# Kernel optimization log

Hardware: AMD Instinct MI355X
Metric: run time of the kernel (lower is better)

The kernel has to match this reference:

```python
import jax, jax.numpy as jnp
import numpy as np

D, H, W = 96, 160, 160
N_FLOWS = 3
RANGE_FLOW = 0.4


def make_base_grid():
    # torch.meshgrid over arange per dim, stacked: [1, 3, D, H, W], channel order (d, h, w)
    zz, yy, xx = jnp.meshgrid(jnp.arange(D), jnp.arange(H), jnp.arange(W), indexing='ij')
    return jnp.stack([zz, yy, xx]).astype(jnp.float32)[None]


def normalize_grid(g):
    # g: [1,3,D,H,W] voxel coords (d,h,w). Apply 2*(v/(s-1) - 0.5), permute to
    # channels-last and reverse channel order -> (x,y,z) as grid_sample expects.
    scale = jnp.array([2.0 / (D - 1), 2.0 / (H - 1), 2.0 / (W - 1)], jnp.float32).reshape(1, 3, 1, 1, 1)
    g = g * scale - 1.0
    return jnp.moveaxis(g, 1, -1)[..., ::-1]  # [1,D,H,W,3], xyz


def grid_sample_3d(img, grid):
    # Trilinear grid_sample, align_corners=False, zeros padding (torch defaults).
    # img: [N,C,D,H,W]; grid: [N,D,H,W,3] with (x,y,z) in [-1,1].
    N, C, Di, Hi, Wi = img.shape
    x = ((grid[..., 0] + 1.0) * Wi - 1.0) * 0.5
    y = ((grid[..., 1] + 1.0) * Hi - 1.0) * 0.5
    z = ((grid[..., 2] + 1.0) * Di - 1.0) * 0.5
    x0 = jnp.floor(x); y0 = jnp.floor(y); z0 = jnp.floor(z)
    tx = x - x0; ty = y - y0; tz = z - z0
    x0i = x0.astype(jnp.int32); y0i = y0.astype(jnp.int32); z0i = z0.astype(jnp.int32)

    gather = jax.vmap(lambda im, a, b, c: im[:, a, b, c])  # per-batch [C,D,H,W] gather

    out = jnp.zeros((N, C) + x.shape[1:], img.dtype)
    for dz in (0, 1):
        for dy in (0, 1):
            for dx in (0, 1):
                xi = x0i + dx; yi = y0i + dy; zi = z0i + dz
                w = ((tx if dx else 1.0 - tx) * (ty if dy else 1.0 - ty) * (tz if dz else 1.0 - tz))
                valid = ((xi >= 0) & (xi < Wi) & (yi >= 0) & (yi < Hi) & (zi >= 0) & (zi < Di))
                xi = jnp.clip(xi, 0, Wi - 1); yi = jnp.clip(yi, 0, Hi - 1); zi = jnp.clip(zi, 0, Di - 1)
                vals = gather(img, zi, yi, xi)  # [N,C,D,H,W]
                out = out + vals * (w * valid)[:, None]
    return out


def setup_inputs() -> dict:
    key = jax.random.key(0)
    k1, k2, k3 = jax.random.split(key, 3)
    src = jax.random.normal(k1, (1, 1, D, H, W), jnp.float32)
    flow_list = jax.random.normal(k2, (N_FLOWS, 1, 3, D, H, W), jnp.float32)
    final_flow = jax.random.normal(k3, (1, 3, D, H, W), jnp.float32)
    range_flow = jnp.float32(RANGE_FLOW)
    return {"src": src, "flow_list": flow_list, "final_flow": final_flow, "range_flow": range_flow}


def reference(src, flow_list, final_flow, range_flow):
    base = make_base_grid()  # [1,3,D,H,W]
    flows = [flow_list[i] for i in range(flow_list.shape[0])] + [final_flow]
    composed = flows[0]
    warped = composed
    for dvf in flows[1:]:
        grid2 = normalize_grid(base + dvf * range_flow)
        warped = grid_sample_3d(composed, grid2)  # warp running composition by dvf
        composed = warped + dvf
    out_flow = warped + final_flow  # == final composed dvf
    new_locs = normalize_grid(base + composed * range_flow)
    deform_2_img = grid_sample_3d(src, new_locs)
    return (deform_2_img, out_flow)
```

## Files before the change

### kernel.cpp

```cpp
#include <hip/hip_runtime.h>

constexpr int Dd  = 96;
constexpr int Hh  = 160;
constexpr int Ww  = 160;
constexpr int HW  = Hh * Ww;
constexpr int DHW = Dd * HW;
constexpr int NBLK  = DHW / 256;
constexpr int CHUNK = NBLK / 8;

__device__ __forceinline__ int swz_block(int b) {
    return (b & 7) * CHUNK + (b >> 3);
}

__device__ __forceinline__ float remap_z(float v) { return v * ((float)Dd / (float)(Dd - 1)) - 0.5f; }
__device__ __forceinline__ float remap_y(float v) { return v * ((float)Hh / (float)(Hh - 1)) - 0.5f; }
__device__ __forceinline__ float remap_x(float v) { return v * ((float)Ww / (float)(Ww - 1)) - 0.5f; }

__device__ __forceinline__ void tri_setup(float x, float y, float z,
                                          int off[8], float wgt[8]) {
    float xf = floorf(x), yf = floorf(y), zf = floorf(z);
    float tx = x - xf, ty = y - yf, tz = z - zf;
    int x0 = (int)xf, y0 = (int)yf, z0 = (int)zf;
    float wx[2] = {1.0f - tx, tx};
    float wy[2] = {1.0f - ty, ty};
    float wz[2] = {1.0f - tz, tz};
    int k = 0;
#pragma unroll
    for (int dz = 0; dz < 2; ++dz) {
        int zi = z0 + dz;
        bool vz = (zi >= 0) && (zi < Dd);
        int zc = min(max(zi, 0), Dd - 1);
#pragma unroll
        for (int dy = 0; dy < 2; ++dy) {
            int yi = y0 + dy;
            bool vy = (yi >= 0) && (yi < Hh);
            int yc = min(max(yi, 0), Hh - 1);
#pragma unroll
            for (int dx = 0; dx < 2; ++dx) {
                int xi = x0 + dx;
                bool vx = (xi >= 0) && (xi < Ww);
                int xc = min(max(xi, 0), Ww - 1);
                float w = wz[dz] * wy[dy] * wx[dx];
                wgt[k] = (vx && vy && vz) ? w : 0.0f;
                off[k] = zc * HW + yc * Ww + xc;
                ++k;
            }
        }
    }
}

__global__ __launch_bounds__(256) void pack3to4(
        const float* __restrict__ f, float4* __restrict__ out)
{
    int idx = blockIdx.x * blockDim.x + threadIdx.x;
    out[idx] = make_float4(f[idx], f[DHW + idx], f[2 * DHW + idx], 0.0f);
}

__global__ __launch_bounds__(256) void warp_compose4(
        const float4* __restrict__ composed,
        const float* __restrict__ dvf,
        const float* __restrict__ rf_ptr,
        float4* __restrict__ out4)
{
    int idx = swz_block(blockIdx.x) * 256 + threadIdx.x;
    float rf = *rf_ptr;

    int d = idx / HW;
    int rem = idx - d * HW;
    int h = rem / Ww;
    int w = rem - h * Ww;

    float fd = dvf[idx];
    float fh = dvf[DHW + idx];
    float fw = dvf[2 * DHW + idx];

    float z = remap_z((float)d + fd * rf);
    float y = remap_y((float)h + fh * rf);
    float x = remap_x((float)w + fw * rf);

    int off[8]; float wgt[8];
    tri_setup(x, y, z, off, wgt);

    float a0 = 0.0f, a1 = 0.0f, a2 = 0.0f;
#pragma unroll
    for (int k = 0; k < 8; ++k) {
        float4 v = composed[off[k]];
        float wk = wgt[k];
        a0 += wk * v.x;
        a1 += wk * v.y;
        a2 += wk * v.z;
    }
    out4[idx] = make_float4(a0 + fd, a1 + fh, a2 + fw, 0.0f);
}

__global__ __launch_bounds__(256) void warp_final_fused(
        const float4* __restrict__ composed2,
        const float* __restrict__ fflow,
        const float* __restrict__ src,
        const float* __restrict__ rf_ptr,
        float* __restrict__ out_flow,
        float* __restrict__ out_img)
{
    int idx = swz_block(blockIdx.x) * 256 + threadIdx.x;
    float rf = *rf_ptr;

    int d = idx / HW;
    int rem = idx - d * HW;
    int h = rem / Ww;
    int w = rem - h * Ww;

    float fd = fflow[idx];
    float fh = fflow[DHW + idx];
    float fw = fflow[2 * DHW + idx];

    float z = remap_z((float)d + fd * rf);
    float y = remap_y((float)h + fh * rf);
    float x = remap_x((float)w + fw * rf);

    int off[8]; float wgt[8];
    tri_setup(x, y, z, off, wgt);

    float a0 = 0.0f, a1 = 0.0f, a2 = 0.0f;
#pragma unroll
    for (int k = 0; k < 8; ++k) {
        float4 v = composed2[off[k]];
        float wk = wgt[k];
        a0 += wk * v.x;
        a1 += wk * v.y;
        a2 += wk * v.z;
    }
    float c0 = a0 + fd, c1 = a1 + fh, c2 = a2 + fw;
    out_flow[idx]           = c0;
    out_flow[DHW + idx]     = c1;
    out_flow[2 * DHW + idx] = c2;

    float z2 = remap_z((float)d + c0 * rf);
    float y2 = remap_y((float)h + c1 * rf);
    float x2 = remap_x((float)w + c2 * rf);

    tri_setup(x2, y2, z2, off, wgt);
    float acc = 0.0f;
#pragma unroll
    for (int k = 0; k < 8; ++k) {
        acc += wgt[k] * src[off[k]];
    }
    out_img[idx] = acc;
}

extern "C" void kernel_launch(void* const* d_in, const int* in_sizes, int n_in,
                              void* d_out, int out_size, void* d_ws, size_t ws_size,
                              hipStream_t stream) {
    const float* src        = (const float*)d_in[0];
    const float* flow_list  = (const float*)d_in[1];
    const float* final_flow = (const float*)d_in[2];
    const float* rf         = (const float*)d_in[3];

    float* out_img  = (float*)d_out;
    float* out_flow = (float*)d_out + DHW;

    float4* bufA = (float4*)d_ws;
    float4* bufB = bufA + DHW;

    const float* f0 = flow_list;
    const float* f1 = flow_list + 3 * (size_t)DHW;
    const float* f2 = flow_list + 6 * (size_t)DHW;

    dim3 block(256);
    dim3 grid(NBLK);

    pack3to4<<<grid, block, 0, stream>>>(f0, bufA);
    warp_compose4<<<grid, block, 0, stream>>>(bufA, f1, rf, bufB);
    warp_compose4<<<grid, block, 0, stream>>>(bufB, f2, rf, bufA);
    warp_final_fused<<<grid, block, 0, stream>>>(bufA, final_flow, src, rf,
                                                 out_flow, out_img);
}
```

Measured before the change: 278.0 us.

## Tile thread blocks as 3D bricks and fold pack kernel into first warp

Thread blocks now cover a 16x8x2 brick of voxels instead of a linear run of 256 voxels, so each block's trilinear gathers touch a more compact neighbourhood and get better cache reuse. The separate pack-to-float4 kernel is removed. The first compose step now gathers straight from the planar input flow with three scalar loads per corner. This saves one launch and a full pass over the flow field, at the cost of less coalesced scalar gathers in the first warp kernel.

```diff
diff --git a/kernel.cpp b/kernel.cpp
--- a/kernel.cpp
+++ b/kernel.cpp
@@ -5,11 +5,25 @@
 constexpr int Ww  = 160;
 constexpr int HW  = Hh * Ww;
 constexpr int DHW = Dd * HW;
-constexpr int NBLK  = DHW / 256;
+
+constexpr int TZ = 2, TY = 8, TX = 16;
+constexpr int NTX = Ww / TX;
+constexpr int NTY = Hh / TY;
+constexpr int NTZ = Dd / TZ;
+constexpr int NBLK = NTX * NTY * NTZ;
 constexpr int CHUNK = NBLK / 8;
 
-__device__ __forceinline__ int swz_block(int b) {
-    return (b & 7) * CHUNK + (b >> 3);
+__device__ __forceinline__ void decode_block(int b, int tid,
+                                             int& z, int& y, int& x, int& idx) {
+    int s = (b & 7) * CHUNK + (b >> 3);
+    int tx = s % NTX;
+    int t2 = s / NTX;
+    int ty = t2 % NTY;
+    int tz = t2 / NTY;
+    x = tx * TX + (tid & 15);
+    y = ty * TY + ((tid >> 4) & 7);
+    z = tz * TZ + (tid >> 7);
+    idx = z * HW + y * Ww + x;
 }
 
 __device__ __forceinline__ float remap_z(float v) { return v * ((float)Dd / (float)(Dd - 1)) - 0.5f; }
@@ -49,37 +63,59 @@
     }
 }
 
-__global__ __launch_bounds__(256) void pack3to4(
-        const float* __restrict__ f, float4* __restrict__ out)
+__global__ __launch_bounds__(256) void warp_compose_p2i(
+        const float* __restrict__ f0,
+        const float* __restrict__ dvf,
+        const float* __restrict__ rf_ptr,
+        float4* __restrict__ out4)
 {
-    int idx = blockIdx.x * blockDim.x + threadIdx.x;
-    out[idx] = make_float4(f[idx], f[DHW + idx], f[2 * DHW + idx], 0.0f);
-}
-
-__global__ __launch_bounds__(256) void warp_compose4(
+    int z, y, x, idx;
+    decode_block(blockIdx.x, threadIdx.x, z, y, x, idx);
+    float rf = *rf_ptr;
+
+    float fd = dvf[idx];
+    float fh = dvf[DHW + idx];
+    float fw = dvf[2 * DHW + idx];
+
+    float zz = remap_z((float)z + fd * rf);
+    float yy = remap_y((float)y + fh * rf);
+    float xx = remap_x((float)x + fw * rf);
+
+    int off[8]; float wgt[8];
+    tri_setup(xx, yy, zz, off, wgt);
+
+    float a0 = 0.0f, a1 = 0.0f, a2 = 0.0f;
+#pragma unroll
+    for (int k = 0; k < 8; ++k) {
+        float wk = wgt[k];
+        int o = off[k];
+        a0 += wk * f0[o];
+        a1 += wk * f0[DHW + o];
+        a2 += wk * f0[2 * DHW + o];
+    }
+    out4[idx] = make_float4(a0 + fd, a1 + fh, a2 + fw, 0.0f);
+}
+
+__global__ __launch_bounds__(256) void warp_compose_i2i(
         const float4* __restrict__ composed,
         const float* __restrict__ dvf,
         const float* __restrict__ rf_ptr,
         float4* __restrict__ out4)
 {
-    int idx = swz_block(blockIdx.x) * 256 + threadIdx.x;
+    int z, y, x, idx;
+    decode_block(blockIdx.x, threadIdx.x, z, y, x, idx);
     float rf = *rf_ptr;
-
-    int d = idx / HW;
-    int rem = idx - d * HW;
-    int h = rem / Ww;
-    int w = rem - h * Ww;
 
     float fd = dvf[idx];
     float fh = dvf[DHW + idx];
     float fw = dvf[2 * DHW + idx];
 
-    float z = remap_z((float)d + fd * rf);
-    float y = remap_y((float)h + fh * rf);
-    float x = remap_x((float)w + fw * rf);
+    float zz = remap_z((float)z + fd * rf);
+    float yy = remap_y((float)y + fh * rf);
+    float xx = remap_x((float)x + fw * rf);
 
     int off[8]; float wgt[8];
-    tri_setup(x, y, z, off, wgt);
+    tri_setup(xx, yy, zz, off, wgt);
 
     float a0 = 0.0f, a1 = 0.0f, a2 = 0.0f;
 #pragma unroll
@@ -101,24 +137,20 @@
         float* __restrict__ out_flow,
         float* __restrict__ out_img)
 {
-    int idx = swz_block(blockIdx.x) * 256 + threadIdx.x;
+    int z, y, x, idx;
+    decode_block(blockIdx.x, threadIdx.x, z, y, x, idx);
     float rf = *rf_ptr;
-
-    int d = idx / HW;
-    int rem = idx - d * HW;
-    int h = rem / Ww;
-    int w = rem - h * Ww;
 
     float fd = fflow[idx];
     float fh = fflow[DHW + idx];
     float fw = fflow[2 * DHW + idx];
 
-    float z = remap_z((float)d + fd * rf);
-    float y = remap_y((float)h + fh * rf);
-    float x = remap_x((float)w + fw * rf);
+    float zz = remap_z((float)z + fd * rf);
+    float yy = remap_y((float)y + fh * rf);
+    float xx = remap_x((float)x + fw * rf);
 
     int off[8]; float wgt[8];
-    tri_setup(x, y, z, off, wgt);
+    tri_setup(xx, yy, zz, off, wgt);
 
     float a0 = 0.0f, a1 = 0.0f, a2 = 0.0f;
 #pragma unroll
@@ -134,9 +166,9 @@
     out_flow[DHW + idx]     = c1;
     out_flow[2 * DHW + idx] = c2;
 
-    float z2 = remap_z((float)d + c0 * rf);
-    float y2 = remap_y((float)h + c1 * rf);
-    float x2 = remap_x((float)w + c2 * rf);
+    float z2 = remap_z((float)z + c0 * rf);
+    float y2 = remap_y((float)y + c1 * rf);
+    float x2 = remap_x((float)x + c2 * rf);
 
     tri_setup(x2, y2, z2, off, wgt);
     float acc = 0.0f;
@@ -168,9 +200,8 @@
     dim3 block(256);
     dim3 grid(NBLK);
 
-    pack3to4<<<grid, block, 0, stream>>>(f0, bufA);
-    warp_compose4<<<grid, block, 0, stream>>>(bufA, f1, rf, bufB);
-    warp_compose4<<<grid, block, 0, stream>>>(bufB, f2, rf, bufA);
+    warp_compose_p2i<<<grid, block, 0, stream>>>(f0, f1, rf, bufB);
+    warp_compose_i2i<<<grid, block, 0, stream>>>(bufB, f2, rf, bufA);
     warp_final_fused<<<grid, block, 0, stream>>>(bufA, final_flow, src, rf,
                                                  out_flow, out_img);
 }
```

Measured after the change: 276.0 us. No clear change (-0.7%).

## Stage 3D halo tiles in LDS for trilinear gathers and fuse pack kernel

Applied to the files above, without the earlier changes.

Switches each warp kernel from per-voxel global gathers to 3D output tiles: a halo region of the source field is cooperatively loaded into shared memory, and trilinear taps are read from LDS whenever the sample falls inside the halo, with a global-memory fallback otherwise. The pack3to4 kernel is removed by reading the first planar flow directly in the first compose pass, saving one launch and one full pass over memory. The costs are halo load overhead, LDS occupancy limits, and divergent fallback paths when displacements exceed the halo margin.

```diff
diff --git a/kernel.cpp b/kernel.cpp
--- a/kernel.cpp
+++ b/kernel.cpp
@@ -5,144 +5,276 @@
 constexpr int Ww  = 160;
 constexpr int HW  = Hh * Ww;
 constexpr int DHW = Dd * HW;
-constexpr int NBLK  = DHW / 256;
-constexpr int CHUNK = NBLK / 8;
-
-__device__ __forceinline__ int swz_block(int b) {
-    return (b & 7) * CHUNK + (b >> 3);
-}
-
-__device__ __forceinline__ float remap_z(float v) { return v * ((float)Dd / (float)(Dd - 1)) - 0.5f; }
-__device__ __forceinline__ float remap_y(float v) { return v * ((float)Hh / (float)(Hh - 1)) - 0.5f; }
-__device__ __forceinline__ float remap_x(float v) { return v * ((float)Ww / (float)(Ww - 1)) - 0.5f; }
-
-__device__ __forceinline__ void tri_setup(float x, float y, float z,
-                                          int off[8], float wgt[8]) {
-    float xf = floorf(x), yf = floorf(y), zf = floorf(z);
-    float tx = x - xf, ty = y - yf, tz = z - zf;
-    int x0 = (int)xf, y0 = (int)yf, z0 = (int)zf;
-    float wx[2] = {1.0f - tx, tx};
-    float wy[2] = {1.0f - ty, ty};
-    float wz[2] = {1.0f - tz, tz};
-    int k = 0;
-#pragma unroll
-    for (int dz = 0; dz < 2; ++dz) {
-        int zi = z0 + dz;
-        bool vz = (zi >= 0) && (zi < Dd);
-        int zc = min(max(zi, 0), Dd - 1);
-#pragma unroll
-        for (int dy = 0; dy < 2; ++dy) {
-            int yi = y0 + dy;
-            bool vy = (yi >= 0) && (yi < Hh);
-            int yc = min(max(yi, 0), Hh - 1);
-#pragma unroll
-            for (int dx = 0; dx < 2; ++dx) {
-                int xi = x0 + dx;
-                bool vx = (xi >= 0) && (xi < Ww);
-                int xc = min(max(xi, 0), Ww - 1);
-                float w = wz[dz] * wy[dy] * wx[dx];
-                wgt[k] = (vx && vy && vz) ? w : 0.0f;
-                off[k] = zc * HW + yc * Ww + xc;
-                ++k;
-            }
-        }
-    }
-}
-
-__global__ __launch_bounds__(256) void pack3to4(
-        const float* __restrict__ f, float4* __restrict__ out)
-{
-    int idx = blockIdx.x * blockDim.x + threadIdx.x;
-    out[idx] = make_float4(f[idx], f[DHW + idx], f[2 * DHW + idx], 0.0f);
-}
-
-__global__ __launch_bounds__(256) void warp_compose4(
-        const float4* __restrict__ composed,
-        const float* __restrict__ dvf,
-        const float* __restrict__ rf_ptr,
+
+constexpr float KZ = 96.0f / 95.0f;
+constexpr float KY = 160.0f / 159.0f;
+constexpr float KX = 160.0f / 159.0f;
+
+constexpr int C_TZ = 4, C_TY = 8, C_TX = 16;
+constexpr int C_SZ = 10, C_SY = 14, C_SX = 22;
+constexpr int C_CELLS = C_SZ * C_SY * C_SX;
+constexpr int C_NTX = Ww / C_TX;
+constexpr int C_NTY = Hh / C_TY;
+constexpr int C_NTZ = Dd / C_TZ;
+constexpr int C_NBLK = C_NTX * C_NTY * C_NTZ;
+constexpr int C_CHUNK = C_NBLK / 8;
+
+constexpr int F_TZ = 2, F_TY = 8, F_TX = 16;
+constexpr int F_SZ = 8,  F_SY = 14, F_SX = 22;
+constexpr int F_CELLS = F_SZ * F_SY * F_SX;
+constexpr int S_SZ = 12, S_SY = 18, S_SX = 26;
+constexpr int S_CELLS = S_SZ * S_SY * S_SX;
+constexpr int F_NTX = Ww / F_TX;
+constexpr int F_NTY = Hh / F_TY;
+constexpr int F_NTZ = Dd / F_TZ;
+constexpr int F_NBLK = F_NTX * F_NTY * F_NTZ;
+constexpr int F_CHUNK = F_NBLK / 8;
+
+__device__ __forceinline__ int iclamp(int v, int lo, int hi) {
+    return min(max(v, lo), hi);
+}
+
+struct Ax { int i0; float w0, w1; };
+__device__ __forceinline__ Ax axis_setup(float s, int n) {
+    float f = floorf(s);
+    int i0 = (int)f;
+    float t = s - f;
+    Ax a;
+    a.i0 = i0;
+    a.w0 = (i0 >= 0 && i0 < n) ? 1.0f - t : 0.0f;
+    a.w1 = (i0 + 1 >= 0 && i0 + 1 < n) ? t : 0.0f;
+    return a;
+}
+
+template <bool PLANAR_SRC>
+__global__ __launch_bounds__(256) void compose_lds(
+        const float4* __restrict__ src4,
+        const float*  __restrict__ srcp,
+        const float*  __restrict__ dvf,
+        const float*  __restrict__ rf_ptr,
         float4* __restrict__ out4)
 {
-    int idx = swz_block(blockIdx.x) * 256 + threadIdx.x;
+    __shared__ float4 sm[C_CELLS];
+
+    int s = (blockIdx.x & 7) * C_CHUNK + (blockIdx.x >> 3);
+    int tx = s % C_NTX; int t2 = s / C_NTX;
+    int ty = t2 % C_NTY; int tz = t2 / C_NTY;
+    int ox = tx * C_TX, oy = ty * C_TY, oz = tz * C_TZ;
+
+    int bx = (int)floorf((float)(ox - 2) * KX - 0.5f);
+    int by = (int)floorf((float)(oy - 2) * KY - 0.5f);
+    int bz = (int)floorf((float)(oz - 2) * KZ - 0.5f);
+
+    for (int c = threadIdx.x; c < C_CELLS; c += 256) {
+        int lx = c % C_SX; int tt = c / C_SX;
+        int ly = tt % C_SY; int lz = tt / C_SY;
+        int gx = iclamp(bx + lx, 0, Ww - 1);
+        int gy = iclamp(by + ly, 0, Hh - 1);
+        int gz = iclamp(bz + lz, 0, Dd - 1);
+        int g = gz * HW + gy * Ww + gx;
+        if (PLANAR_SRC)
+            sm[c] = make_float4(srcp[g], srcp[DHW + g], srcp[2 * DHW + g], 0.0f);
+        else
+            sm[c] = src4[g];
+    }
+    __syncthreads();
+
     float rf = *rf_ptr;
-
-    int d = idx / HW;
-    int rem = idx - d * HW;
-    int h = rem / Ww;
-    int w = rem - h * Ww;
-
-    float fd = dvf[idx];
-    float fh = dvf[DHW + idx];
-    float fw = dvf[2 * DHW + idx];
-
-    float z = remap_z((float)d + fd * rf);
-    float y = remap_y((float)h + fh * rf);
-    float x = remap_x((float)w + fw * rf);
-
-    int off[8]; float wgt[8];
-    tri_setup(x, y, z, off, wgt);
-
-    float a0 = 0.0f, a1 = 0.0f, a2 = 0.0f;
-#pragma unroll
-    for (int k = 0; k < 8; ++k) {
-        float4 v = composed[off[k]];
-        float wk = wgt[k];
-        a0 += wk * v.x;
-        a1 += wk * v.y;
-        a2 += wk * v.z;
-    }
-    out4[idx] = make_float4(a0 + fd, a1 + fh, a2 + fw, 0.0f);
-}
-
-__global__ __launch_bounds__(256) void warp_final_fused(
+    int vx  = ox + (threadIdx.x & 15);
+    int vy  = oy + ((threadIdx.x >> 4) & 7);
+    int vz0 = oz + (threadIdx.x >> 7);
+
+#pragma unroll
+    for (int rep = 0; rep < 2; ++rep) {
+        int vz = vz0 + rep * 2;
+        int idx = vz * HW + vy * Ww + vx;
+
+        float fd = dvf[idx];
+        float fh = dvf[DHW + idx];
+        float fw = dvf[2 * DHW + idx];
+
+        Ax az = axis_setup(((float)vz + fd * rf) * KZ - 0.5f, Dd);
+        Ax ay = axis_setup(((float)vy + fh * rf) * KY - 0.5f, Hh);
+        Ax ax = axis_setup(((float)vx + fw * rf) * KX - 0.5f, Ww);
+
+        float wz[2] = {az.w0, az.w1};
+        float wy[2] = {ay.w0, ay.w1};
+        float wx[2] = {ax.w0, ax.w1};
+
+        int lz = az.i0 - bz, ly = ay.i0 - by, lx = ax.i0 - bx;
+        bool ok = (unsigned)lz <= (unsigned)(C_SZ - 2) &&
+                  (unsigned)ly <= (unsigned)(C_SY - 2) &&
+                  (unsigned)lx <= (unsigned)(C_SX - 2);
+
+        float a0 = 0.0f, a1 = 0.0f, a2 = 0.0f;
+        if (ok) {
+#pragma unroll
+            for (int dz = 0; dz < 2; ++dz)
+#pragma unroll
+                for (int dy = 0; dy < 2; ++dy)
+#pragma unroll
+                    for (int dx = 0; dx < 2; ++dx) {
+                        float wk = wz[dz] * wy[dy] * wx[dx];
+                        float4 v = sm[((lz + dz) * C_SY + (ly + dy)) * C_SX + lx + dx];
+                        a0 += wk * v.x; a1 += wk * v.y; a2 += wk * v.z;
+                    }
+        } else {
+            int cz[2] = {iclamp(az.i0, 0, Dd - 1), iclamp(az.i0 + 1, 0, Dd - 1)};
+            int cy[2] = {iclamp(ay.i0, 0, Hh - 1), iclamp(ay.i0 + 1, 0, Hh - 1)};
+            int cx[2] = {iclamp(ax.i0, 0, Ww - 1), iclamp(ax.i0 + 1, 0, Ww - 1)};
+#pragma unroll
+            for (int dz = 0; dz < 2; ++dz)
+#pragma unroll
+                for (int dy = 0; dy < 2; ++dy)
+#pragma unroll
+                    for (int dx = 0; dx < 2; ++dx) {
+                        float wk = wz[dz] * wy[dy] * wx[dx];
+                        int g = cz[dz] * HW + cy[dy] * Ww + cx[dx];
+                        if (PLANAR_SRC) {
+                            a0 += wk * srcp[g];
+                            a1 += wk * srcp[DHW + g];
+                            a2 += wk * srcp[2 * DHW + g];
+                        } else {
+                            float4 v = src4[g];
+                            a0 += wk * v.x; a1 += wk * v.y; a2 += wk * v.z;
+                        }
+                    }
+        }
+        out4[idx] = make_float4(a0 + fd, a1 + fh, a2 + fw, 0.0f);
+    }
+}
+
+__global__ __launch_bounds__(256) void final_fused_lds(
         const float4* __restrict__ composed2,
-        const float* __restrict__ fflow,
-        const float* __restrict__ src,
-        const float* __restrict__ rf_ptr,
+        const float*  __restrict__ fflow,
+        const float*  __restrict__ src,
+        const float*  __restrict__ rf_ptr,
         float* __restrict__ out_flow,
         float* __restrict__ out_img)
 {
-    int idx = swz_block(blockIdx.x) * 256 + threadIdx.x;
+    __shared__ float4 smc[F_CELLS];
+    __shared__ float  sms[S_CELLS];
+
+    int s = (blockIdx.x & 7) * F_CHUNK + (blockIdx.x >> 3);
+    int tx = s % F_NTX; int t2 = s / F_NTX;
+    int ty = t2 % F_NTY; int tz = t2 / F_NTY;
+    int ox = tx * F_TX, oy = ty * F_TY, oz = tz * F_TZ;
+
+    int bx = (int)floorf((float)(ox - 2) * KX - 0.5f);
+    int by = (int)floorf((float)(oy - 2) * KY - 0.5f);
+    int bz = (int)floorf((float)(oz - 2) * KZ - 0.5f);
+    int b2x = (int)floorf((float)(ox - 4) * KX - 0.5f);
+    int b2y = (int)floorf((float)(oy - 4) * KY - 0.5f);
+    int b2z = (int)floorf((float)(oz - 4) * KZ - 0.5f);
+
+    for (int c = threadIdx.x; c < F_CELLS; c += 256) {
+        int lx = c % F_SX; int tt = c / F_SX;
+        int ly = tt % F_SY; int lz = tt / F_SY;
+        int gx = iclamp(bx + lx, 0, Ww - 1);
+        int gy = iclamp(by + ly, 0, Hh - 1);
+        int gz = iclamp(bz + lz, 0, Dd - 1);
+        smc[c] = composed2[gz * HW + gy * Ww + gx];
+    }
+    for (int c = threadIdx.x; c < S_CELLS; c += 256) {
+        int lx = c % S_SX; int tt = c / S_SX;
+        int ly = tt % S_SY; int lz = tt / S_SY;
+        int gx = iclamp(b2x + lx, 0, Ww - 1);
+        int gy = iclamp(b2y + ly, 0, Hh - 1);
+        int gz = iclamp(b2z + lz, 0, Dd - 1);
+        sms[c] = src[gz * HW + gy * Ww + gx];
+    }
+    __syncthreads();
+
     float rf = *rf_ptr;
-
-    int d = idx / HW;
-    int rem = idx - d * HW;
-    int h = rem / Ww;
-    int w = rem - h * Ww;
+    int vx = ox + (threadIdx.x & 15);
+    int vy = oy + ((threadIdx.x >> 4) & 7);
+    int vz = oz + (threadIdx.x >> 7);
+    int idx = vz * HW + vy * Ww + vx;
 
     float fd = fflow[idx];
     float fh = fflow[DHW + idx];
     float fw = fflow[2 * DHW + idx];
 
-    float z = remap_z((float)d + fd * rf);
-    float y = remap_y((float)h + fh * rf);
-    float x = remap_x((float)w + fw * rf);
-
-    int off[8]; float wgt[8];
-    tri_setup(x, y, z, off, wgt);
+    Ax az = axis_setup(((float)vz + fd * rf) * KZ - 0.5f, Dd);
+    Ax ay = axis_setup(((float)vy + fh * rf) * KY - 0.5f, Hh);
+    Ax ax = axis_setup(((float)vx + fw * rf) * KX - 0.5f, Ww);
+    float wz[2] = {az.w0, az.w1};
+    float wy[2] = {ay.w0, ay.w1};
+    float wx[2] = {ax.w0, ax.w1};
+
+    int lz = az.i0 - bz, ly = ay.i0 - by, lx = ax.i0 - bx;
+    bool ok = (unsigned)lz <= (unsigned)(F_SZ - 2) &&
+              (unsigned)ly <= (unsigned)(F_SY - 2) &&
+              (unsigned)lx <= (unsigned)(F_SX - 2);
 
     float a0 = 0.0f, a1 = 0.0f, a2 = 0.0f;
-#pragma unroll
-    for (int k = 0; k < 8; ++k) {
-        float4 v = composed2[off[k]];
-        float wk = wgt[k];
-        a0 += wk * v.x;
-        a1 += wk * v.y;
-        a2 += wk * v.z;
+    if (ok) {
+#pragma unroll
+        for (int dz = 0; dz < 2; ++dz)
+#pragma unroll
+            for (int dy = 0; dy < 2; ++dy)
+#pragma unroll
+                for (int dx = 0; dx < 2; ++dx) {
+                    float wk = wz[dz] * wy[dy] * wx[dx];
+                    float4 v = smc[((lz + dz) * F_SY + (ly + dy)) * F_SX + lx + dx];
+                    a0 += wk * v.x; a1 += wk * v.y; a2 += wk * v.z;
+                }
+    } else {
+        int cz[2] = {iclamp(az.i0, 0, Dd - 1), iclamp(az.i0 + 1, 0, Dd - 1)};
+        int cy[2] = {iclamp(ay.i0, 0, Hh - 1), iclamp(ay.i0 + 1, 0, Hh - 1)};
+        int cx[2] = {iclamp(ax.i0, 0, Ww - 1), iclamp(ax.i0 + 1, 0, Ww - 1)};
+#pragma unroll
+        for (int dz = 0; dz < 2; ++dz)
+#pragma unroll
+            for (int dy = 0; dy < 2; ++dy)
+#pragma unroll
+                for (int dx = 0; dx < 2; ++dx) {
+                    float wk = wz[dz] * wy[dy] * wx[dx];
+                    float4 v = composed2[cz[dz] * HW + cy[dy] * Ww + cx[dx]];
+                    a0 += wk * v.x; a1 += wk * v.y; a2 += wk * v.z;
+                }
     }
     float c0 = a0 + fd, c1 = a1 + fh, c2 = a2 + fw;
     out_flow[idx]           = c0;
     out_flow[DHW + idx]     = c1;
     out_flow[2 * DHW + idx] = c2;
 
-    float z2 = remap_z((float)d + c0 * rf);
-    float y2 = remap_y((float)h + c1 * rf);
-    float x2 = remap_x((float)w + c2 * rf);
-
-    tri_setup(x2, y2, z2, off, wgt);
+    Ax sz_ = axis_setup(((float)vz + c0 * rf) * KZ - 0.5f, Dd);
+    Ax sy_ = axis_setup(((float)vy + c1 * rf) * KY - 0.5f, Hh);
+    Ax sx_ = axis_setup(((float)vx + c2 * rf) * KX - 0.5f, Ww);
+    float uz[2] = {sz_.w0, sz_.w1};
+    float uy[2] = {sy_.w0, sy_.w1};
+    float ux[2] = {sx_.w0, sx_.w1};
+
+    int mz = sz_.i0 - b2z, my = sy_.i0 - b2y, mx = sx_.i0 - b2x;
+    bool ok2 = (unsigned)mz <= (unsigned)(S_SZ - 2) &&
+               (unsigned)my <= (unsigned)(S_SY - 2) &&
+               (unsigned)mx <= (unsigned)(S_SX - 2);
+
     float acc = 0.0f;
-#pragma unroll
-    for (int k = 0; k < 8; ++k) {
-        acc += wgt[k] * src[off[k]];
+    if (ok2) {
+#pragma unroll
+        for (int dz = 0; dz < 2; ++dz)
+#pragma unroll
+            for (int dy = 0; dy < 2; ++dy)
+#pragma unroll
+                for (int dx = 0; dx < 2; ++dx) {
+                    float wk = uz[dz] * uy[dy] * ux[dx];
+                    acc += wk * sms[((mz + dz) * S_SY + (my + dy)) * S_SX + mx + dx];
+                }
+    } else {
+        int cz[2] = {iclamp(sz_.i0, 0, Dd - 1), iclamp(sz_.i0 + 1, 0, Dd - 1)};
+        int cy[2] = {iclamp(sy_.i0, 0, Hh - 1), iclamp(sy_.i0 + 1, 0, Hh - 1)};
+        int cx[2] = {iclamp(sx_.i0, 0, Ww - 1), iclamp(sx_.i0 + 1, 0, Ww - 1)};
+#pragma unroll
+        for (int dz = 0; dz < 2; ++dz)
+#pragma unroll
+            for (int dy = 0; dy < 2; ++dy)
+#pragma unroll
+                for (int dx = 0; dx < 2; ++dx) {
+                    float wk = uz[dz] * uy[dy] * ux[dx];
+                    acc += wk * src[cz[dz] * HW + cy[dy] * Ww + cx[dx]];
+                }
     }
     out_img[idx] = acc;
 }
@@ -166,11 +298,9 @@
     const float* f2 = flow_list + 6 * (size_t)DHW;
 
     dim3 block(256);
-    dim3 grid(NBLK);
-
-    pack3to4<<<grid, block, 0, stream>>>(f0, bufA);
-    warp_compose4<<<grid, block, 0, stream>>>(bufA, f1, rf, bufB);
-    warp_compose4<<<grid, block, 0, stream>>>(bufB, f2, rf, bufA);
-    warp_final_fused<<<grid, block, 0, stream>>>(bufA, final_flow, src, rf,
-                                                 out_flow, out_img);
-}
+
+    compose_lds<true><<<dim3(C_NBLK), block, 0, stream>>>(nullptr, f0, f1, rf, bufB);
+    compose_lds<false><<<dim3(C_NBLK), block, 0, stream>>>(bufB, nullptr, f2, rf, bufA);
+    final_fused_lds<<<dim3(F_NBLK), block, 0, stream>>>(bufA, final_flow, src, rf,
+                                                        out_flow, out_img);
+}
```

Result: slower. 474.0 us (+70.5%).
